# Kernel tuning notes

Measured on AMD Instinct MI355X. Metric: run time of the kernel, lower is better.

The kernel has to match this reference:

```python
import jax, jax.numpy as jnp
import numpy as np

M0, M1 = 32, 16          # multiplicities of 0e (scalars) and 1o (vectors)
FEAT = M0 + 3 * M1       # 80
WNUM = M0*M0 + M1*M1 + M0*M1 + M1*M0  # 2304 per-edge TP weights
N_NODES, N_EDGES, N_RBF, HID = 10000, 160000, 50, 64
EPS = 1e-5
INV_SQRT3 = 1.0 / np.sqrt(3.0)
# per-path normalization: 1/sqrt(num_paths_to_output * mul_in)
A_P1 = 1.0 / np.sqrt(2.0 * M0)   # 0e x 0e -> 0e
A_P4 = 1.0 / np.sqrt(2.0 * M1)   # 1o x 1o -> 0e
A_P2 = 1.0 / np.sqrt(2.0 * M1)   # 1o x 0e -> 1o
A_P3 = 1.0 / np.sqrt(2.0 * M0)   # 0e x 1o -> 1o


def setup_inputs() -> dict:
    key = jax.random.key(0)
    ks = jax.random.split(key, 12)
    def lin(k, fi, fo):
        return jax.random.normal(k, (fi, fo), jnp.float32) / np.sqrt(fi)
    return dict(
        h=jax.random.normal(ks[0], (N_NODES, FEAT), jnp.float32),
        edge_index=jax.random.randint(ks[1], (2, N_EDGES), 0, N_NODES),
        edge_sh=jax.random.normal(ks[2], (N_EDGES, 4), jnp.float32),
        edge_features=jax.random.normal(ks[3], (N_EDGES, N_RBF), jnp.float32),
        W1e=lin(ks[4], N_RBF, HID), b1e=jnp.zeros(HID, jnp.float32),
        W2e=lin(ks[5], HID, HID), b2e=jnp.zeros(HID, jnp.float32),
        W3e=lin(ks[6], HID, WNUM) * 0.1, b3e=jnp.zeros(WNUM, jnp.float32),
        A0=jax.random.normal(ks[7], (M0, M0), jnp.float32),
        A1p=jax.random.normal(ks[8], (M1, M1), jnp.float32),
        bn_w0=jnp.ones(M0, jnp.float32), bn_b0=jnp.zeros(M0, jnp.float32),
        bn_w1=jnp.ones(M1, jnp.float32),
    )


def _forward(h, edge_index, edge_sh, edge_features,
             W1e, b1e, W2e, b2e, W3e, b3e, A0, A1p, bn_w0, bn_b0, bn_w1):
    N = h.shape[0]
    E = edge_sh.shape[0]
    src, dst = edge_index[0], edge_index[1]

    # ---- edge MLP -> per-edge tensor-product weights [E, WNUM] ----
    w = jax.nn.silu(edge_features @ W1e + b1e)
    w = jax.nn.silu(w @ W2e + b2e)
    w = w @ W3e + b3e
    o1 = M0 * M0
    o2 = o1 + M1 * M1
    o3 = o2 + M0 * M1
    w1 = w[:, :o1].reshape(E, M0, M0)     # 0e x 0e -> 0e
    w2 = w[:, o1:o2].reshape(E, M1, M1)   # 1o x 0e -> 1o
    w3 = w[:, o2:o3].reshape(E, M0, M1)   # 0e x 1o -> 1o
    w4 = w[:, o3:].reshape(E, M1, M0)     # 1o x 1o -> 0e

    # ---- gather source node features ----
    s0 = h[src, :M0]                         # [E, M0]
    s1 = h[src, M0:].reshape(E, M1, 3)       # [E, M1, 3]
    y0 = edge_sh[:, 0]                       # [E]
    y1 = edge_sh[:, 1:4]                     # [E, 3]

    # ---- fully connected tensor product with per-edge weights ----
    # scalar output: 0e x 0e -> 0e  and  1o x 1o -> 0e (dot / sqrt(3))
    dot11 = jnp.einsum('eui,ei->eu', s1, y1) * INV_SQRT3      # [E, M1]
    m0 = (A_P1 * jnp.einsum('eu,euw->ew', s0 * y0[:, None], w1)
          + A_P4 * jnp.einsum('eu,euw->ew', dot11, w4))       # [E, M0]
    # vector output: 1o x 0e -> 1o  and  0e x 1o -> 1o
    m1 = (A_P2 * jnp.einsum('eui,euw->ewi', s1 * y0[:, None, None], w2)
          + A_P3 * jnp.einsum('eu,ei,euw->ewi', s0, y1, w3))  # [E, M1, 3]
    messages = jnp.concatenate([m0, m1.reshape(E, 3 * M1)], axis=1)  # [E, FEAT]

    # ---- scatter-mean aggregation to destination nodes ----
    agg = jax.ops.segment_sum(messages, dst, num_segments=N)
    cnt = jax.ops.segment_sum(jnp.ones((E,), messages.dtype), dst, num_segments=N)
    agg = agg / jnp.maximum(cnt, 1.0)[:, None]

    # ---- equivariant self-interaction (per-l linear mixing) ----
    self0 = (h[:, :M0] @ A0) / np.sqrt(M0)
    h1 = h[:, M0:].reshape(N, M1, 3)
    self1 = jnp.einsum('nui,uw->nwi', h1, A1p) / np.sqrt(M1)
    out = agg + jnp.concatenate([self0, self1.reshape(N, 3 * M1)], axis=1)

    # ---- equivariant batch norm (layer mode) ----
    x0 = out[:, :M0]
    x1 = out[:, M0:].reshape(N, M1, 3)
    mu = x0.mean(axis=0)
    var = x0.var(axis=0)
    x0n = (x0 - mu) * jax.lax.rsqrt(var + EPS) * bn_w0 + bn_b0
    nrm2 = (x1 ** 2).sum(axis=-1).mean(axis=0)               # [M1]
    x1n = x1 * (jax.lax.rsqrt(nrm2 + EPS) * bn_w1)[None, :, None]
    out = jnp.concatenate([x0n, x1n.reshape(N, 3 * M1)], axis=1)

    # ---- residual (irreps_in == irreps_out) ----
    return out + h


def reference(h, edge_index, edge_sh, edge_features,
              W1e, b1e, W2e, b2e, W3e, b3e, A0, A1p, bn_w0, bn_b0, bn_w1):
    return _forward(h, edge_index, edge_sh, edge_features,
                    W1e, b1e, W2e, b2e, W3e, b3e, A0, A1p, bn_w0, bn_b0, bn_w1)
```

## Files before the change

kernel.cpp:

```cpp
#include <hip/hip_runtime.h>
#include <math.h>

#define NN 10000
#define NE 160000
#define NRBF 50
#define WNUM 2304
#define EPSV 1e-5f

#define A_P1 0.125f
#define A_P2 0.17677669529663687f
#define A_P3 0.125f
#define A_P4 0.17677669529663687f
#define INV_SQRT3 0.5773502691896258f
#define INV_SQRT_M0 0.17677669529663687f
#define INV_SQRT_M1 0.25f

typedef __attribute__((ext_vector_type(8))) short bf16x8;
typedef __attribute__((ext_vector_type(4))) float f32x4;
typedef __attribute__((ext_vector_type(4))) int i32x4;

#define MFMA16(a, b, c) __builtin_amdgcn_mfma_f32_16x16x32_bf16(a, b, c, 0, 0, 0)

__device__ __forceinline__ short f2bf(float x) {
  unsigned u = __float_as_uint(x);
  unsigned r = (u + 0x7fffu + ((u >> 16) & 1u)) >> 16;
  return (short)r;
}

__global__ void prep_weights(const float* __restrict__ W1, const float* __restrict__ W2,
                             const float* __restrict__ W3, short* __restrict__ W1P,
                             short* __restrict__ W2P, short* __restrict__ W3P) {
  int s = blockIdx.x * 256 + threadIdx.x;
  if (s < WNUM * 64) {
    int t = s >> 10, r = s & 1023;
    int ch = r >> 9, l = (r >> 3) & 63, kk = r & 7;
    int row = t * 16 + (l & 15);
    int k = ((l >> 4) << 3) + (ch << 5) + kk;
    W3P[s] = f2bf(W3[k * WNUM + row]);
  } else if (s < WNUM * 64 + 4096) {
    int s2 = s - WNUM * 64;
    int t = s2 >> 10, r = s2 & 1023;
    int ch = r >> 9, l = (r >> 3) & 63, kk = r & 7;
    int row = t * 16 + (l & 15);
    int k = ((l >> 4) << 3) + (ch << 5) + kk;
    W1P[s2] = f2bf(k < NRBF ? W1[k * 64 + row] : 0.f);
  } else if (s < WNUM * 64 + 8192) {
    int s2 = s - WNUM * 64 - 4096;
    int t = s2 >> 10, r = s2 & 1023;
    int ch = r >> 9, l = (r >> 3) & 63, kk = r & 7;
    int row = t * 16 + (l & 15);
    int k = ((l >> 4) << 3) + (ch << 5) + kk;
    W2P[s2] = f2bf(W2[k * 64 + row]);
  }
}

#define TILE_V(JT, V)                                         \
  {                                                           \
    const short* wb = W3P + ((JT) << 10) + (l << 3);          \
    bf16x8 b0 = *(const bf16x8*)wb;                           \
    bf16x8 b1f = *(const bf16x8*)(wb + 512);                  \
    float bias = b3[((JT) << 4) + lr];                        \
    f32x4 d = {bias, bias, bias, bias};                       \
    d = MFMA16(a0, b0, d);                                    \
    V = MFMA16(a1, b1f, d);                                   \
  }

__global__ __launch_bounds__(256, 3) void edge_kernel(
    const float* __restrict__ h, const int* __restrict__ eidx,
    const float* __restrict__ esh, const float* __restrict__ ef,
    const short* __restrict__ W1P, const float* __restrict__ b1,
    const short* __restrict__ W2P, const float* __restrict__ b2,
    const short* __restrict__ W3P, const float* __restrict__ b3,
    float* __restrict__ agg, float* __restrict__ cnt) {
  __shared__ short buf0[64 * 72];
  __shared__ short h1s[64 * 72];
  __shared__ float a0s[32 * 64];
  __shared__ float s0c[32 * 64];
  __shared__ float cYs[3 * 16 * 64];
  __shared__ float d4s[16 * 64];
  __shared__ float y1s[3 * 64];
  __shared__ float b1s[64], b2s[64];
  __shared__ int dsts[64];

  const int tid = threadIdx.x;
  const int e0 = blockIdx.x * 64;

  for (int idx = tid; idx < 64 * 64; idx += 256) {
    int e = idx >> 6, k = idx & 63;
    float v = (k < NRBF) ? ef[(long)(e0 + e) * NRBF + k] : 0.f;
    buf0[e * 72 + k] = f2bf(v);
  }
  if (tid < 64) { b1s[tid] = b1[tid]; b2s[tid] = b2[tid]; }
  {
    int e = tid >> 2, q = tid & 3;
    int ge = e0 + e;
    int src = eidx[ge];
    float y0 = esh[ge * 4 + 0];
    float y1x = esh[ge * 4 + 1], y1y = esh[ge * 4 + 2], y1z = esh[ge * 4 + 3];
    const float* hs = h + (long)src * 80;
    for (int u = q; u < 32; u += 4) {
      float s = hs[u];
      a0s[u * 64 + e] = A_P1 * y0 * s;
      s0c[u * 64 + e] = A_P3 * s;
    }
    for (int u = q; u < 16; u += 4) {
      float sx = hs[32 + u * 3], sy = hs[33 + u * 3], sz = hs[34 + u * 3];
      cYs[(0 * 16 + u) * 64 + e] = A_P2 * y0 * sx;
      cYs[(1 * 16 + u) * 64 + e] = A_P2 * y0 * sy;
      cYs[(2 * 16 + u) * 64 + e] = A_P2 * y0 * sz;
      d4s[u * 64 + e] = A_P4 * INV_SQRT3 * (sx * y1x + sy * y1y + sz * y1z);
    }
    if (q == 0) {
      y1s[0 * 64 + e] = y1x; y1s[1 * 64 + e] = y1y; y1s[2 * 64 + e] = y1z;
      dsts[e] = eidx[NE + ge];
    }
  }
  __syncthreads();

  const int wid = tid >> 6, l = tid & 63;
  const int er = wid * 16;
  const int lr = l & 15, lg = l >> 4;
  const int row4 = er + lg * 4;

  {
    bf16x8 a0 = *(const bf16x8*)&buf0[(er + lr) * 72 + lg * 8];
    bf16x8 a1 = *(const bf16x8*)&buf0[(er + lr) * 72 + 32 + lg * 8];
#pragma unroll
    for (int jt = 0; jt < 4; ++jt) {
      const short* wb = W1P + (jt << 10) + (l << 3);
      bf16x8 b0 = *(const bf16x8*)wb;
      bf16x8 b1f = *(const bf16x8*)(wb + 512);
      float bias = b1s[jt * 16 + lr];
      f32x4 d = {bias, bias, bias, bias};
      d = MFMA16(a0, b0, d);
      d = MFMA16(a1, b1f, d);
#pragma unroll
      for (int r = 0; r < 4; ++r) {
        float x = d[r];
        x = x / (1.f + __expf(-x));
        h1s[(row4 + r) * 72 + jt * 16 + lr] = f2bf(x);
      }
    }
  }
  __syncthreads();

  {
    bf16x8 a0 = *(const bf16x8*)&h1s[(er + lr) * 72 + lg * 8];
    bf16x8 a1 = *(const bf16x8*)&h1s[(er + lr) * 72 + 32 + lg * 8];
#pragma unroll
    for (int jt = 0; jt < 4; ++jt) {
      const short* wb = W2P + (jt << 10) + (l << 3);
      bf16x8 b0 = *(const bf16x8*)wb;
      bf16x8 b1f = *(const bf16x8*)(wb + 512);
      float bias = b2s[jt * 16 + lr];
      f32x4 d = {bias, bias, bias, bias};
      d = MFMA16(a0, b0, d);
      d = MFMA16(a1, b1f, d);
#pragma unroll
      for (int r = 0; r < 4; ++r) {
        float x = d[r];
        x = x / (1.f + __expf(-x));
        buf0[(row4 + r) * 72 + jt * 16 + lr] = f2bf(x);
      }
    }
  }
  __syncthreads();

  bf16x8 a0 = *(const bf16x8*)&buf0[(er + lr) * 72 + lg * 8];
  bf16x8 a1 = *(const bf16x8*)&buf0[(er + lr) * 72 + 32 + lg * 8];
  f32x4 y1r0 = *(const f32x4*)&y1s[0 * 64 + row4];
  f32x4 y1r1 = *(const f32x4*)&y1s[1 * 64 + row4];
  f32x4 y1r2 = *(const f32x4*)&y1s[2 * 64 + row4];
  i32x4 dd = *(const i32x4*)&dsts[row4];

  f32x4 m0f0 = {0.f, 0.f, 0.f, 0.f}, m0f1 = {0.f, 0.f, 0.f, 0.f};
  f32x4 m1f0 = {0.f, 0.f, 0.f, 0.f}, m1f1 = {0.f, 0.f, 0.f, 0.f},
        m1f2 = {0.f, 0.f, 0.f, 0.f};

#pragma unroll 2
  for (int jp = 0; jp < 32; ++jp) {
    f32x4 c = *(const f32x4*)&a0s[jp * 64 + row4];
    f32x4 v, v2;
    TILE_V(jp * 2, v);
    TILE_V(jp * 2 + 1, v2);
#pragma unroll
    for (int r = 0; r < 4; ++r) {
      m0f0[r] += c[r] * v[r];
      m0f1[r] += c[r] * v2[r];
    }
  }

#pragma unroll 4
  for (int u = 0; u < 16; ++u) {
    f32x4 v;
    TILE_V(64 + u, v);
    f32x4 c0 = *(const f32x4*)&cYs[(0 * 16 + u) * 64 + row4];
    f32x4 c1 = *(const f32x4*)&cYs[(1 * 16 + u) * 64 + row4];
    f32x4 c2 = *(const f32x4*)&cYs[(2 * 16 + u) * 64 + row4];
#pragma unroll
    for (int r = 0; r < 4; ++r) {
      m1f0[r] += c0[r] * v[r];
      m1f1[r] += c1[r] * v[r];
      m1f2[r] += c2[r] * v[r];
    }
  }

#pragma unroll 4
  for (int u = 0; u < 32; ++u) {
    f32x4 v;
    TILE_V(80 + u, v);
    f32x4 c = *(const f32x4*)&s0c[u * 64 + row4];
#pragma unroll
    for (int r = 0; r < 4; ++r) {
      float t = c[r] * v[r];
      m1f0[r] += t * y1r0[r];
      m1f1[r] += t * y1r1[r];
      m1f2[r] += t * y1r2[r];
    }
  }

#pragma unroll 2
  for (int up = 0; up < 16; ++up) {
    f32x4 c = *(const f32x4*)&d4s[up * 64 + row4];
    f32x4 v, v2;
    TILE_V(112 + up * 2, v);
    TILE_V(112 + up * 2 + 1, v2);
#pragma unroll
    for (int r = 0; r < 4; ++r) {
      m0f0[r] += c[r] * v[r];
      m0f1[r] += c[r] * v2[r];
    }
  }

#pragma unroll
  for (int r = 0; r < 4; ++r) {
    float* base = agg + (long)dd[r] * 80;
    atomicAdd(base + lr, m0f0[r]);
    atomicAdd(base + 16 + lr, m0f1[r]);
    atomicAdd(base + 32 + lr * 3 + 0, m1f0[r]);
    atomicAdd(base + 32 + lr * 3 + 1, m1f1[r]);
    atomicAdd(base + 32 + lr * 3 + 2, m1f2[r]);
  }
  if (tid < 64) atomicAdd(cnt + dsts[tid], 1.0f);
}

__global__ __launch_bounds__(256) void node_a(
    const float* __restrict__ h, const float* __restrict__ A0,
    const float* __restrict__ A1p, const float* __restrict__ agg,
    const float* __restrict__ cnt, float* __restrict__ outpre,
    float* __restrict__ stats) {
  __shared__ float redw[4][80];
  const int tid = threadIdx.x;
  const int wid = tid >> 6, l = tid & 63;
  const int n = blockIdx.x * 256 + tid;
  float x0[32], x1[48];
#pragma unroll
  for (int w = 0; w < 32; w++) x0[w] = 0.f;
#pragma unroll
  for (int c = 0; c < 48; c++) x1[c] = 0.f;
  if (n < NN) {
    const float* hr = h + (long)n * 80;
    const float* ar = agg + (long)n * 80;
    float inv = 1.f / fmaxf(cnt[n], 1.f);
#pragma unroll 1
    for (int u = 0; u < 32; u++) {
      float hu = hr[u];
#pragma unroll
      for (int w = 0; w < 32; w++) x0[w] += hu * A0[u * 32 + w];
    }
#pragma unroll
    for (int w = 0; w < 32; w++) x0[w] = x0[w] * INV_SQRT_M0 + ar[w] * inv;
#pragma unroll 1
    for (int u = 0; u < 16; u++) {
      float a = hr[32 + u * 3], b_ = hr[33 + u * 3], c_ = hr[34 + u * 3];
#pragma unroll
      for (int w = 0; w < 16; w++) {
        float Aw = A1p[u * 16 + w];
        x1[w * 3 + 0] += a * Aw;
        x1[w * 3 + 1] += b_ * Aw;
        x1[w * 3 + 2] += c_ * Aw;
      }
    }
#pragma unroll
    for (int c = 0; c < 48; c++) x1[c] = x1[c] * INV_SQRT_M1 + ar[32 + c] * inv;
    float* opr = outpre + (long)n * 80;
#pragma unroll
    for (int w = 0; w < 32; w++) opr[w] = x0[w];
#pragma unroll
    for (int c = 0; c < 48; c++) opr[32 + c] = x1[c];
  }
#pragma unroll 1
  for (int c = 0; c < 32; ++c) {
    float s = x0[c];
#pragma unroll
    for (int m = 32; m >= 1; m >>= 1) s += __shfl_xor(s, m, 64);
    if (l == 0) redw[wid][c] = s;
  }
#pragma unroll 1
  for (int c = 0; c < 32; ++c) {
    float v = x0[c];
    float s = v * v;
#pragma unroll
    for (int m = 32; m >= 1; m >>= 1) s += __shfl_xor(s, m, 64);
    if (l == 0) redw[wid][32 + c] = s;
  }
#pragma unroll 1
  for (int u = 0; u < 16; ++u) {
    float s = x1[u * 3] * x1[u * 3] + x1[u * 3 + 1] * x1[u * 3 + 1] +
              x1[u * 3 + 2] * x1[u * 3 + 2];
#pragma unroll
    for (int m = 32; m >= 1; m >>= 1) s += __shfl_xor(s, m, 64);
    if (l == 0) redw[wid][64 + u] = s;
  }
  __syncthreads();
  if (tid < 80)
    atomicAdd(&stats[tid],
              redw[0][tid] + redw[1][tid] + redw[2][tid] + redw[3][tid]);
}

__global__ void node_b(const float* __restrict__ outpre, const float* __restrict__ stats,
                       const float* __restrict__ bnw0, const float* __restrict__ bnb0,
                       const float* __restrict__ bnw1, const float* __restrict__ h,
                       float* __restrict__ out) {
  int idx = blockIdx.x * 256 + threadIdx.x;
  if (idx >= NN * 80) return;
  int c = idx % 80;
  float v = outpre[idx];
  const float invN = 1.f / NN;
  float o;
  if (c < 32) {
    float mu = stats[c] * invN;
    float var = stats[32 + c] * invN - mu * mu;
    o = (v - mu) * rsqrtf(var + EPSV) * bnw0[c] + bnb0[c];
  } else {
    int u = (c - 32) / 3;
    float nr = stats[64 + u] * invN;
    o = v * rsqrtf(nr + EPSV) * bnw1[u];
  }
  out[idx] = o + h[idx];
}

extern "C" void kernel_launch(void* const* d_in, const int* in_sizes, int n_in,
                              void* d_out, int out_size, void* d_ws, size_t ws_size,
                              hipStream_t stream) {
  const float* h    = (const float*)d_in[0];
  const int*   eidx = (const int*)d_in[1];
  const float* esh  = (const float*)d_in[2];
  const float* ef   = (const float*)d_in[3];
  const float* W1   = (const float*)d_in[4];
  const float* b1   = (const float*)d_in[5];
  const float* W2   = (const float*)d_in[6];
  const float* b2   = (const float*)d_in[7];
  const float* W3   = (const float*)d_in[8];
  const float* b3   = (const float*)d_in[9];
  const float* A0   = (const float*)d_in[10];
  const float* A1p  = (const float*)d_in[11];
  const float* bnw0 = (const float*)d_in[12];
  const float* bnb0 = (const float*)d_in[13];
  const float* bnw1 = (const float*)d_in[14];
  float* out = (float*)d_out;

  float* ws = (float*)d_ws;
  float* agg    = ws;
  float* cnt    = ws + 800000;
  float* stats  = ws + 810000;
  float* outpre = ws + 810080;
  short* W3P    = (short*)(ws + 1610080);
  short* W1P    = W3P + WNUM * 64;
  short* W2P    = W1P + 4096;

  hipMemsetAsync(agg, 0, (size_t)810080 * sizeof(float), stream);

  prep_weights<<<(WNUM * 64 + 8192 + 255) / 256, 256, 0, stream>>>(W1, W2, W3, W1P,
                                                                   W2P, W3P);
  edge_kernel<<<NE / 64, 256, 0, stream>>>(h, eidx, esh, ef, W1P, b1, W2P, b2, W3P, b3,
                                           agg, cnt);
  node_a<<<(NN + 255) / 256, 256, 0, stream>>>(h, A0, A1p, agg, cnt, outpre, stats);
  node_b<<<(NN * 80 + 255) / 256, 256, 0, stream>>>(outpre, stats, bnw0, bnb0, bnw1, h,
                                                    out);
}
```

Before: 234.7 us.

## Split W3 output tiles across waves so each weight fragment serves all edges

```diff
diff --git a/kernel.cpp b/kernel.cpp
--- a/kernel.cpp
+++ b/kernel.cpp
@@ -54,33 +54,19 @@
   }
 }
 
-#define TILE_V(JT, V)                                         \
-  {                                                           \
-    const short* wb = W3P + ((JT) << 10) + (l << 3);          \
-    bf16x8 b0 = *(const bf16x8*)wb;                           \
-    bf16x8 b1f = *(const bf16x8*)(wb + 512);                  \
-    float bias = b3[((JT) << 4) + lr];                        \
-    f32x4 d = {bias, bias, bias, bias};                       \
-    d = MFMA16(a0, b0, d);                                    \
-    V = MFMA16(a1, b1f, d);                                   \
-  }
-
-__global__ __launch_bounds__(256, 3) void edge_kernel(
+__global__ __launch_bounds__(256, 4) void edge_kernel(
     const float* __restrict__ h, const int* __restrict__ eidx,
     const float* __restrict__ esh, const float* __restrict__ ef,
     const short* __restrict__ W1P, const float* __restrict__ b1,
     const short* __restrict__ W2P, const float* __restrict__ b2,
     const short* __restrict__ W3P, const float* __restrict__ b3,
     float* __restrict__ agg, float* __restrict__ cnt) {
-  __shared__ short buf0[64 * 72];
-  __shared__ short h1s[64 * 72];
-  __shared__ float a0s[32 * 64];
-  __shared__ float s0c[32 * 64];
-  __shared__ float cYs[3 * 16 * 64];
-  __shared__ float d4s[16 * 64];
-  __shared__ float y1s[3 * 64];
+  __shared__ short act[64 * 72];
+  __shared__ float coef[6144];
+  __shared__ float y0s[64], y1s[192];
   __shared__ float b1s[64], b2s[64];
   __shared__ int dsts[64];
+  float* scratch = coef;
 
   const int tid = threadIdx.x;
   const int e0 = blockIdx.x * 64;
@@ -88,7 +74,7 @@
   for (int idx = tid; idx < 64 * 64; idx += 256) {
     int e = idx >> 6, k = idx & 63;
     float v = (k < NRBF) ? ef[(long)(e0 + e) * NRBF + k] : 0.f;
-    buf0[e * 72 + k] = f2bf(v);
+    act[e * 72 + k] = f2bf(v);
   }
   if (tid < 64) { b1s[tid] = b1[tid]; b2s[tid] = b2[tid]; }
   {
@@ -98,33 +84,30 @@
     float y0 = esh[ge * 4 + 0];
     float y1x = esh[ge * 4 + 1], y1y = esh[ge * 4 + 2], y1z = esh[ge * 4 + 3];
     const float* hs = h + (long)src * 80;
-    for (int u = q; u < 32; u += 4) {
-      float s = hs[u];
-      a0s[u * 64 + e] = A_P1 * y0 * s;
-      s0c[u * 64 + e] = A_P3 * s;
-    }
+    for (int u = q; u < 32; u += 4) coef[u * 64 + e] = 0.125f * hs[u];
     for (int u = q; u < 16; u += 4) {
       float sx = hs[32 + u * 3], sy = hs[33 + u * 3], sz = hs[34 + u * 3];
-      cYs[(0 * 16 + u) * 64 + e] = A_P2 * y0 * sx;
-      cYs[(1 * 16 + u) * 64 + e] = A_P2 * y0 * sy;
-      cYs[(2 * 16 + u) * 64 + e] = A_P2 * y0 * sz;
-      d4s[u * 64 + e] = A_P4 * INV_SQRT3 * (sx * y1x + sy * y1y + sz * y1z);
+      coef[2048 + u * 64 + e] = A_P2 * sx;
+      coef[3072 + u * 64 + e] = A_P2 * sy;
+      coef[4096 + u * 64 + e] = A_P2 * sz;
+      coef[5120 + u * 64 + e] = A_P4 * INV_SQRT3 * (sx * y1x + sy * y1y + sz * y1z);
     }
     if (q == 0) {
-      y1s[0 * 64 + e] = y1x; y1s[1 * 64 + e] = y1y; y1s[2 * 64 + e] = y1z;
+      y0s[e] = y0;
+      y1s[e] = y1x; y1s[64 + e] = y1y; y1s[128 + e] = y1z;
       dsts[e] = eidx[NE + ge];
     }
   }
   __syncthreads();
 
   const int wid = tid >> 6, l = tid & 63;
+  const int lr = l & 15, lg = l >> 4;
+  const int g16 = lg * 4;
   const int er = wid * 16;
-  const int lr = l & 15, lg = l >> 4;
-  const int row4 = er + lg * 4;
 
   {
-    bf16x8 a0 = *(const bf16x8*)&buf0[(er + lr) * 72 + lg * 8];
-    bf16x8 a1 = *(const bf16x8*)&buf0[(er + lr) * 72 + 32 + lg * 8];
+    bf16x8 a0 = *(const bf16x8*)&act[(er + lr) * 72 + lg * 8];
+    bf16x8 a1 = *(const bf16x8*)&act[(er + lr) * 72 + 32 + lg * 8];
 #pragma unroll
     for (int jt = 0; jt < 4; ++jt) {
       const short* wb = W1P + (jt << 10) + (l << 3);
@@ -138,15 +121,13 @@
       for (int r = 0; r < 4; ++r) {
         float x = d[r];
         x = x / (1.f + __expf(-x));
-        h1s[(row4 + r) * 72 + jt * 16 + lr] = f2bf(x);
-      }
-    }
-  }
-  __syncthreads();
-
+        act[(er + lg * 4 + r) * 72 + jt * 16 + lr] = f2bf(x);
+      }
+    }
+  }
   {
-    bf16x8 a0 = *(const bf16x8*)&h1s[(er + lr) * 72 + lg * 8];
-    bf16x8 a1 = *(const bf16x8*)&h1s[(er + lr) * 72 + 32 + lg * 8];
+    bf16x8 a0 = *(const bf16x8*)&act[(er + lr) * 72 + lg * 8];
+    bf16x8 a1 = *(const bf16x8*)&act[(er + lr) * 72 + 32 + lg * 8];
 #pragma unroll
     for (int jt = 0; jt < 4; ++jt) {
       const short* wb = W2P + (jt << 10) + (l << 3);
@@ -160,88 +141,211 @@
       for (int r = 0; r < 4; ++r) {
         float x = d[r];
         x = x / (1.f + __expf(-x));
-        buf0[(row4 + r) * 72 + jt * 16 + lr] = f2bf(x);
+        act[(er + lg * 4 + r) * 72 + jt * 16 + lr] = f2bf(x);
       }
     }
   }
   __syncthreads();
 
-  bf16x8 a0 = *(const bf16x8*)&buf0[(er + lr) * 72 + lg * 8];
-  bf16x8 a1 = *(const bf16x8*)&buf0[(er + lr) * 72 + 32 + lg * 8];
-  f32x4 y1r0 = *(const f32x4*)&y1s[0 * 64 + row4];
-  f32x4 y1r1 = *(const f32x4*)&y1s[1 * 64 + row4];
-  f32x4 y1r2 = *(const f32x4*)&y1s[2 * 64 + row4];
-  i32x4 dd = *(const i32x4*)&dsts[row4];
-
-  f32x4 m0f0 = {0.f, 0.f, 0.f, 0.f}, m0f1 = {0.f, 0.f, 0.f, 0.f};
-  f32x4 m1f0 = {0.f, 0.f, 0.f, 0.f}, m1f1 = {0.f, 0.f, 0.f, 0.f},
-        m1f2 = {0.f, 0.f, 0.f, 0.f};
-
-#pragma unroll 2
-  for (int jp = 0; jp < 32; ++jp) {
-    f32x4 c = *(const f32x4*)&a0s[jp * 64 + row4];
-    f32x4 v, v2;
-    TILE_V(jp * 2, v);
-    TILE_V(jp * 2 + 1, v2);
+  bf16x8 a0g[4], a1g[4];
+#pragma unroll
+  for (int g = 0; g < 4; ++g) {
+    a0g[g] = *(const bf16x8*)&act[(g * 16 + lr) * 72 + lg * 8];
+    a1g[g] = *(const bf16x8*)&act[(g * 16 + lr) * 72 + 32 + lg * 8];
+  }
+
+#define M0_PAIR(TE, COFF)                                            \
+  {                                                                  \
+    const short* wbE = W3P + ((TE) << 10) + (l << 3);                \
+    const short* wbO = W3P + (((TE) + 1) << 10) + (l << 3);          \
+    bf16x8 E0 = *(const bf16x8*)wbE;                                 \
+    bf16x8 E1 = *(const bf16x8*)(wbE + 512);                         \
+    bf16x8 O0 = *(const bf16x8*)wbO;                                 \
+    bf16x8 O1 = *(const bf16x8*)(wbO + 512);                         \
+    float be = b3[((TE) << 4) + lr];                                 \
+    float bo = b3[(((TE) + 1) << 4) + lr];                           \
+    _Pragma("unroll")                                                \
+    for (int g = 0; g < 4; ++g) {                                    \
+      f32x4 c = *(const f32x4*)&coef[(COFF) + g * 16 + g16];         \
+      f32x4 d = {be, be, be, be};                                    \
+      d = MFMA16(a0g[g], E0, d);                                     \
+      f32x4 v = MFMA16(a1g[g], E1, d);                               \
+      f32x4 d2 = {bo, bo, bo, bo};                                   \
+      d2 = MFMA16(a0g[g], O0, d2);                                   \
+      f32x4 v2 = MFMA16(a1g[g], O1, d2);                             \
+      _Pragma("unroll")                                              \
+      for (int r = 0; r < 4; ++r) {                                  \
+        acc0[g][r] += c[r] * v[r];                                   \
+        acc1[g][r] += c[r] * v2[r];                                  \
+      }                                                              \
+    }                                                                \
+  }
+
+#define W2_TILE(U)                                                   \
+  {                                                                  \
+    const short* wb = W3P + ((64 + (U)) << 10) + (l << 3);           \
+    bf16x8 B0 = *(const bf16x8*)wb;                                  \
+    bf16x8 B1 = *(const bf16x8*)(wb + 512);                          \
+    float bb = b3[((64 + (U)) << 4) + lr];                           \
+    _Pragma("unroll")                                                \
+    for (int g = 0; g < 4; ++g) {                                    \
+      f32x4 d = {bb, bb, bb, bb};                                    \
+      d = MFMA16(a0g[g], B0, d);                                     \
+      f32x4 v = MFMA16(a1g[g], B1, d);                               \
+      f32x4 cx = *(const f32x4*)&coef[2048 + (U) * 64 + g * 16 + g16]; \
+      f32x4 cy = *(const f32x4*)&coef[3072 + (U) * 64 + g * 16 + g16]; \
+      f32x4 cz = *(const f32x4*)&coef[4096 + (U) * 64 + g * 16 + g16]; \
+      _Pragma("unroll")                                              \
+      for (int r = 0; r < 4; ++r) {                                  \
+        mx[g][r] += cx[r] * v[r];                                    \
+        my[g][r] += cy[r] * v[r];                                    \
+        mz[g][r] += cz[r] * v[r];                                    \
+      }                                                              \
+    }                                                                \
+  }
+
+#define W3_TILE(U)                                                   \
+  {                                                                  \
+    const short* wb = W3P + ((80 + (U)) << 10) + (l << 3);           \
+    bf16x8 B0 = *(const bf16x8*)wb;                                  \
+    bf16x8 B1 = *(const bf16x8*)(wb + 512);                          \
+    float bb = b3[((80 + (U)) << 4) + lr];                           \
+    _Pragma("unroll")                                                \
+    for (int g = 0; g < 4; ++g) {                                    \
+      f32x4 d = {bb, bb, bb, bb};                                    \
+      d = MFMA16(a0g[g], B0, d);                                     \
+      f32x4 v = MFMA16(a1g[g], B1, d);                               \
+      f32x4 c = *(const f32x4*)&coef[(U) * 64 + g * 16 + g16];       \
+      _Pragma("unroll")                                              \
+      for (int r = 0; r < 4; ++r) t3[g][r] += c[r] * v[r];           \
+    }                                                                \
+  }
+
+  if (wid < 2) {
+    f32x4 acc0[4], acc1[4];
+#pragma unroll
+    for (int g = 0; g < 4; ++g) {
+      acc0[g] = (f32x4){0, 0, 0, 0};
+      acc1[g] = (f32x4){0, 0, 0, 0};
+    }
+    if (wid == 0) {
+#pragma unroll 2
+      for (int u = 0; u < 24; ++u) M0_PAIR(2 * u, u * 64);
+#pragma unroll
+      for (int g = 0; g < 4; ++g) {
+        f32x4 y0v = *(const f32x4*)&y0s[g * 16 + g16];
+#pragma unroll
+        for (int r = 0; r < 4; ++r) { acc0[g][r] *= y0v[r]; acc1[g][r] *= y0v[r]; }
+      }
+    } else {
+#pragma unroll 2
+      for (int u = 24; u < 32; ++u) M0_PAIR(2 * u, u * 64);
+#pragma unroll
+      for (int g = 0; g < 4; ++g) {
+        f32x4 y0v = *(const f32x4*)&y0s[g * 16 + g16];
+#pragma unroll
+        for (int r = 0; r < 4; ++r) { acc0[g][r] *= y0v[r]; acc1[g][r] *= y0v[r]; }
+      }
+#pragma unroll 2
+      for (int p = 0; p < 16; ++p) M0_PAIR(112 + 2 * p, 5120 + p * 64);
+    }
+    __syncthreads();
+    if (wid == 1) {
+      float* p = scratch + l * 20;
+      *(f32x4*)(p + 0) = acc0[0]; *(f32x4*)(p + 4) = acc1[0];
+      *(f32x4*)(p + 8) = acc0[1]; *(f32x4*)(p + 12) = acc1[1];
+    } else {
+      float* p = scratch + 1280 + l * 20;
+      *(f32x4*)(p + 0) = acc0[2]; *(f32x4*)(p + 4) = acc1[2];
+      *(f32x4*)(p + 8) = acc0[3]; *(f32x4*)(p + 12) = acc1[3];
+    }
+    __syncthreads();
+    const int gb = (wid == 0) ? 0 : 2;
+    const float* p = (wid == 0) ? (scratch + l * 20) : (scratch + 1280 + l * 20);
+    f32x4 t0 = *(const f32x4*)(p + 0), t1 = *(const f32x4*)(p + 4);
+    f32x4 t2 = *(const f32x4*)(p + 8), t3_ = *(const f32x4*)(p + 12);
+    i32x4 dd0 = *(const i32x4*)&dsts[(gb + 0) * 16 + g16];
+    i32x4 dd1 = *(const i32x4*)&dsts[(gb + 1) * 16 + g16];
 #pragma unroll
     for (int r = 0; r < 4; ++r) {
-      m0f0[r] += c[r] * v[r];
-      m0f1[r] += c[r] * v2[r];
-    }
-  }
-
-#pragma unroll 4
-  for (int u = 0; u < 16; ++u) {
-    f32x4 v;
-    TILE_V(64 + u, v);
-    f32x4 c0 = *(const f32x4*)&cYs[(0 * 16 + u) * 64 + row4];
-    f32x4 c1 = *(const f32x4*)&cYs[(1 * 16 + u) * 64 + row4];
-    f32x4 c2 = *(const f32x4*)&cYs[(2 * 16 + u) * 64 + row4];
+      float* base = agg + (long)dd0[r] * 80;
+      atomicAdd(base + lr, acc0[gb + 0][r] + t0[r]);
+      atomicAdd(base + 16 + lr, acc1[gb + 0][r] + t1[r]);
+    }
 #pragma unroll
     for (int r = 0; r < 4; ++r) {
-      m1f0[r] += c0[r] * v[r];
-      m1f1[r] += c1[r] * v[r];
-      m1f2[r] += c2[r] * v[r];
-    }
-  }
-
-#pragma unroll 4
-  for (int u = 0; u < 32; ++u) {
-    f32x4 v;
-    TILE_V(80 + u, v);
-    f32x4 c = *(const f32x4*)&s0c[u * 64 + row4];
+      float* base = agg + (long)dd1[r] * 80;
+      atomicAdd(base + lr, acc0[gb + 1][r] + t2[r]);
+      atomicAdd(base + 16 + lr, acc1[gb + 1][r] + t3_[r]);
+    }
+  } else {
+    f32x4 mx[4], my[4], mz[4], t3[4];
+#pragma unroll
+    for (int g = 0; g < 4; ++g) {
+      mx[g] = (f32x4){0, 0, 0, 0}; my[g] = (f32x4){0, 0, 0, 0};
+      mz[g] = (f32x4){0, 0, 0, 0}; t3[g] = (f32x4){0, 0, 0, 0};
+    }
+    if (wid == 2) {
+#pragma unroll 2
+      for (int u = 0; u < 8; ++u) W2_TILE(u);
+#pragma unroll 2
+      for (int u = 0; u < 16; ++u) W3_TILE(u);
+    } else {
+#pragma unroll 2
+      for (int u = 8; u < 16; ++u) W2_TILE(u);
+#pragma unroll 2
+      for (int u = 16; u < 32; ++u) W3_TILE(u);
+    }
+#pragma unroll
+    for (int g = 0; g < 4; ++g) {
+      f32x4 y0v = *(const f32x4*)&y0s[g * 16 + g16];
+      f32x4 yx = *(const f32x4*)&y1s[g * 16 + g16];
+      f32x4 yy = *(const f32x4*)&y1s[64 + g * 16 + g16];
+      f32x4 yz = *(const f32x4*)&y1s[128 + g * 16 + g16];
+#pragma unroll
+      for (int r = 0; r < 4; ++r) {
+        mx[g][r] = mx[g][r] * y0v[r] + yx[r] * t3[g][r];
+        my[g][r] = my[g][r] * y0v[r] + yy[r] * t3[g][r];
+        mz[g][r] = mz[g][r] * y0v[r] + yz[r] * t3[g][r];
+      }
+    }
+    __syncthreads();
+    if (wid == 3) {
+      float* p = scratch + 2560 + l * 28;
+      *(f32x4*)(p + 0) = mx[0]; *(f32x4*)(p + 4) = my[0]; *(f32x4*)(p + 8) = mz[0];
+      *(f32x4*)(p + 12) = mx[1]; *(f32x4*)(p + 16) = my[1]; *(f32x4*)(p + 20) = mz[1];
+    } else {
+      float* p = scratch + 4352 + l * 28;
+      *(f32x4*)(p + 0) = mx[2]; *(f32x4*)(p + 4) = my[2]; *(f32x4*)(p + 8) = mz[2];
+      *(f32x4*)(p + 12) = mx[3]; *(f32x4*)(p + 16) = my[3]; *(f32x4*)(p + 20) = mz[3];
+    }
+    __syncthreads();
+    const int gb = (wid == 2) ? 0 : 2;
+    const float* p = (wid == 2) ? (scratch + 2560 + l * 28) : (scratch + 4352 + l * 28);
+    f32x4 u0 = *(const f32x4*)(p + 0), u1 = *(const f32x4*)(p + 4);
+    f32x4 u2 = *(const f32x4*)(p + 8), u3 = *(const f32x4*)(p + 12);
+    f32x4 u4 = *(const f32x4*)(p + 16), u5 = *(const f32x4*)(p + 20);
+    i32x4 dd0 = *(const i32x4*)&dsts[(gb + 0) * 16 + g16];
+    i32x4 dd1 = *(const i32x4*)&dsts[(gb + 1) * 16 + g16];
 #pragma unroll
     for (int r = 0; r < 4; ++r) {
-      float t = c[r] * v[r];
-      m1f0[r] += t * y1r0[r];
-      m1f1[r] += t * y1r1[r];
-      m1f2[r] += t * y1r2[r];
-    }
-  }
-
-#pragma unroll 2
-  for (int up = 0; up < 16; ++up) {
-    f32x4 c = *(const f32x4*)&d4s[up * 64 + row4];
-    f32x4 v, v2;
-    TILE_V(112 + up * 2, v);
-    TILE_V(112 + up * 2 + 1, v2);
+      float* base = agg + (long)dd0[r] * 80;
+      atomicAdd(base + 32 + lr * 3 + 0, mx[gb + 0][r] + u0[r]);
+      atomicAdd(base + 32 + lr * 3 + 1, my[gb + 0][r] + u1[r]);
+      atomicAdd(base + 32 + lr * 3 + 2, mz[gb + 0][r] + u2[r]);
+    }
 #pragma unroll
     for (int r = 0; r < 4; ++r) {
-      m0f0[r] += c[r] * v[r];
-      m0f1[r] += c[r] * v2[r];
-    }
-  }
-
-#pragma unroll
-  for (int r = 0; r < 4; ++r) {
-    float* base = agg + (long)dd[r] * 80;
-    atomicAdd(base + lr, m0f0[r]);
-    atomicAdd(base + 16 + lr, m0f1[r]);
-    atomicAdd(base + 32 + lr * 3 + 0, m1f0[r]);
-    atomicAdd(base + 32 + lr * 3 + 1, m1f1[r]);
-    atomicAdd(base + 32 + lr * 3 + 2, m1f2[r]);
+      float* base = agg + (long)dd1[r] * 80;
+      atomicAdd(base + 32 + lr * 3 + 0, mx[gb + 1][r] + u3[r]);
+      atomicAdd(base + 32 + lr * 3 + 1, my[gb + 1][r] + u4[r]);
+      atomicAdd(base + 32 + lr * 3 + 2, mz[gb + 1][r] + u5[r]);
+    }
   }
   if (tid < 64) atomicAdd(cnt + dsts[tid], 1.0f);
+#undef M0_PAIR
+#undef W2_TILE
+#undef W3_TILE
 }
 
 __global__ __launch_bounds__(256) void node_a(
```

New measurement: 226.6 us. -3.4%, faster.
